# Kernel tuning notes

Hardware: AMD Instinct MI355X
Metric: run time of the kernel (lower is better)

Reference implementation:

```python
import jax, jax.numpy as jnp
import numpy as np

EPS = 1e-8

def div_small(a, b):
    b_safe = b * (b > EPS) + (b <= EPS) * EPS
    return a / b_safe

def cos_full(q1h, q2h, w):
    # q1h [b,s1,h], q2h [b,s1_or_1,h], w [P,h] -> [b,s1,P]
    a = q1h[:, :, None, :] * w          # [b,s1,P,h]
    c = q2h[:, :, None, :] * w          # [b,s1|1,P,h]
    num = jnp.sum(a * c, axis=-1)
    den = jnp.maximum(jnp.linalg.norm(a, axis=-1) * jnp.linalg.norm(c, axis=-1), EPS)
    return num / den

def cos_maxpool(q1h, q2h, w):
    # q1h [b,s1,h], q2h [b,s2,h], w [P,h] -> max over s2 of cosine -> [b,s1,P]
    a = q1h[:, :, None, :] * w          # [b,s1,P,h]
    c = q2h[:, :, None, :] * w          # [b,s2,P,h]
    num = jnp.einsum('biph,bjph->bijp', a, c)            # [b,s1,s2,P]
    na = jnp.linalg.norm(a, axis=-1)                     # [b,s1,P]
    nc = jnp.linalg.norm(c, axis=-1)                     # [b,s2,P]
    den = jnp.maximum(na[:, :, None, :] * nc[:, None, :, :], EPS)
    return jnp.max(num / den, axis=2)

def attention(q1, q2):
    # cosine-similarity matrix [b,s1,s2]
    n1 = jnp.linalg.norm(q1, axis=2, keepdims=True)      # [b,s1,1]
    n2 = jnp.linalg.norm(q2, axis=2, keepdims=True)      # [b,s2,1]
    num = jnp.einsum('bih,bjh->bij', q1, q2)
    return div_small(num, n1 * jnp.swapaxes(n2, 1, 2))

def setup_inputs() -> dict:
    key = jax.random.key(0)
    k1, k2, kw = jax.random.split(key, 3)
    q1_batch = jax.random.normal(k1, (16, 128, 512), dtype=jnp.float32)
    q2_batch = jax.random.normal(k2, (16, 128, 512), dtype=jnp.float32)
    W = jax.random.normal(kw, (8, 16, 256), dtype=jnp.float32)
    return {"q1_batch": q1_batch, "q2_batch": q2_batch, "W": W}

def reference(q1_batch, q2_batch, W):
    h = q1_batch.shape[-1] // 2
    q1_fw, q1_bw = q1_batch[..., :h], q1_batch[..., h:]
    q2_fw, q2_bw = q2_batch[..., :h], q2_batch[..., h:]

    # 1) full matching against last (fw) / first (bw) q2 state
    full_fw = cos_full(q1_fw, q2_fw[:, -1:, :], W[0])
    full_bw = cos_full(q1_bw, q2_bw[:, :1, :], W[1])

    # 2) max-pool matching over all q2 positions
    max_fw = cos_maxpool(q1_fw, q2_fw, W[2])
    max_bw = cos_maxpool(q1_bw, q2_bw, W[3])

    # 3) attentive matching
    att_fw = attention(q1_fw, q2_fw)                     # [b,s1,s2]
    att_bw = attention(q1_bw, q2_bw)
    at_q2_fw = att_fw[..., None] * q2_fw[:, None, :, :]  # [b,s1,s2,h]
    at_q2_bw = att_bw[..., None] * q2_bw[:, None, :, :]
    mean_fw = div_small(at_q2_fw.sum(axis=2), att_fw.sum(axis=2, keepdims=True))
    # NOTE: denominator intentionally uses att_fw (bug preserved from source)
    mean_bw = div_small(at_q2_bw.sum(axis=2), att_fw.sum(axis=2, keepdims=True))
    attn_fw = cos_full(q1_fw, mean_fw, W[4])
    attn_bw = cos_full(q1_bw, mean_bw, W[5])

    # 4) max-attentive matching
    max_at_fw = at_q2_fw.max(axis=2)                     # [b,s1,h]
    max_at_bw = at_q2_bw.max(axis=2)
    maxattn_fw = cos_full(q1_fw, max_at_fw, W[6])
    maxattn_bw = cos_full(q1_bw, max_at_bw, W[7])

    return jnp.concatenate(
        [full_fw, full_bw, max_fw, max_bw, attn_fw, attn_bw, maxattn_fw, maxattn_bw],
        axis=-1)
```

## Files before the change

kernel.cpp:

```cpp
#include <hip/hip_runtime.h>
#include <hip/hip_bf16.h>

#define B 16
#define L 128
#define H 256
#define H2 512
#define P 16
#define EPSF 1e-8f
#define LDSTR 72
#define PADQ 260
#define PATT 132

typedef __attribute__((ext_vector_type(8))) short short8;
typedef __attribute__((ext_vector_type(4))) short short4v;
typedef __attribute__((ext_vector_type(4))) float f32x4;

__device__ __forceinline__ short f2bf(float x) {
    unsigned u = __builtin_bit_cast(unsigned, x);
    u += 0x7fffu + ((u >> 16) & 1u);
    return (short)(u >> 16);
}
__device__ __forceinline__ float bf2f(short s) {
    unsigned u = ((unsigned)(unsigned short)s) << 16;
    return __builtin_bit_cast(float, u);
}

__global__ void __launch_bounds__(512) k_fused(
        const float* __restrict__ q1, const float* __restrict__ q2,
        const float* __restrict__ W, float* __restrict__ out) {
    int bd = blockIdx.x;
    int b = bd >> 1, dir = bd & 1;
    int m0 = blockIdx.y * 16;
    int t = threadIdx.x;
    int wave = t >> 6, l = t & 63, q = l >> 4, coll = l & 15;

    __shared__ __align__(16) short As[16 * LDSTR];
    __shared__ __align__(16) short Bs[128 * LDSTR];
    __shared__ __align__(16) float att_s[16][PATT];
    __shared__ __align__(16) float meanS[16][PADQ];
    __shared__ __align__(16) float maxS[16][PADQ];
    __shared__ __align__(16) float cful[256];
    __shared__ float nA[16], nB[128];

    const float* q1b = q1 + ((size_t)b * L + m0) * H2 + dir * H;
    const float* q2b = q2 + (size_t)b * L * H2 + dir * H;

    f32x4 acc = (f32x4){0.f, 0.f, 0.f, 0.f};
    float normA = 0.f, normB = 0.f;
    int arow = t >> 4, acol = (t & 15) * 4;
    int brow = t >> 2, bc0 = (t & 3) * 16;

    for (int kt = 0; kt < 4; kt++) {
        int k0 = kt * 64;
        if (t < 256) {
            float4 va = *(const float4*)(q1b + (size_t)arow * H2 + k0 + acol);
            normA += va.x * va.x + va.y * va.y + va.z * va.z + va.w * va.w;
            short4v sa = { f2bf(va.x), f2bf(va.y), f2bf(va.z), f2bf(va.w) };
            *(short4v*)(As + arow * LDSTR + acol) = sa;
        }
        for (int cc = 0; cc < 4; cc++) {
            float4 vb = *(const float4*)(q2b + (size_t)brow * H2 + k0 + bc0 + cc * 4);
            normB += vb.x * vb.x + vb.y * vb.y + vb.z * vb.z + vb.w * vb.w;
            short4v sb = { f2bf(vb.x), f2bf(vb.y), f2bf(vb.z), f2bf(vb.w) };
            *(short4v*)(Bs + brow * LDSTR + bc0 + cc * 4) = sb;
        }
        __syncthreads();
        for (int ks = 0; ks < 2; ks++) {
            int koff = ks * 32 + q * 8;
            short8 af = *(const short8*)(As + coll * LDSTR + koff);
            short8 bf = *(const short8*)(Bs + (wave * 16 + coll) * LDSTR + koff);
            acc = __builtin_amdgcn_mfma_f32_16x16x32_bf16(af, bf, acc, 0, 0, 0);
        }
        __syncthreads();
    }
    if (t < 256) {
        float sA = normA;
        for (int off = 1; off < 16; off <<= 1) sA += __shfl_xor(sA, off, 16);
        if ((t & 15) == 0) nA[arow] = sqrtf(sA);
    }
    {
        float sB = normB;
        sB += __shfl_xor(sB, 1, 4);
        sB += __shfl_xor(sB, 2, 4);
        if ((t & 3) == 0) nB[brow] = sqrtf(sB);
    }
    __syncthreads();
    {
        float n2 = nB[wave * 16 + coll];
        for (int r = 0; r < 4; r++) {
            float den = nA[q * 4 + r] * n2;
            den = den > EPSF ? den : EPSF;
            att_s[q * 4 + r][wave * 16 + coll] = acc[r] / den;
        }
    }
    if (t < 256) cful[t] = q2b[(size_t)(dir ? 0 : (L - 1)) * H2 + t];
    __syncthreads();

    int ig = t >> 6, hq = t & 63;
    int ia = ig * 2, ib = ia + 1;
    f32x4 s0 = (f32x4){0.f, 0.f, 0.f, 0.f}, s1 = s0;
    f32x4 mx0 = (f32x4){-INFINITY, -INFINITY, -INFINITY, -INFINITY}, mx1 = mx0;
    for (int j = 0; j < 128; j += 2) {
        float4 c0 = *(const float4*)(q2b + (size_t)j * H2 + hq * 4);
        float4 c1 = *(const float4*)(q2b + (size_t)(j + 1) * H2 + hq * 4);
        float wa0 = att_s[ia][j],     wb0 = att_s[ib][j];
        float wa1 = att_s[ia][j + 1], wb1 = att_s[ib][j + 1];
        f32x4 v0 = (f32x4){ wa0 * c0.x, wa0 * c0.y, wa0 * c0.z, wa0 * c0.w };
        f32x4 v1 = (f32x4){ wb0 * c0.x, wb0 * c0.y, wb0 * c0.z, wb0 * c0.w };
        f32x4 v2 = (f32x4){ wa1 * c1.x, wa1 * c1.y, wa1 * c1.z, wa1 * c1.w };
        f32x4 v3 = (f32x4){ wb1 * c1.x, wb1 * c1.y, wb1 * c1.z, wb1 * c1.w };
        s0 += v0; s0 += v2;
        s1 += v1; s1 += v3;
        mx0[0] = fmaxf(mx0[0], fmaxf(v0[0], v2[0]));
        mx0[1] = fmaxf(mx0[1], fmaxf(v0[1], v2[1]));
        mx0[2] = fmaxf(mx0[2], fmaxf(v0[2], v2[2]));
        mx0[3] = fmaxf(mx0[3], fmaxf(v0[3], v2[3]));
        mx1[0] = fmaxf(mx1[0], fmaxf(v1[0], v3[0]));
        mx1[1] = fmaxf(mx1[1], fmaxf(v1[1], v3[1]));
        mx1[2] = fmaxf(mx1[2], fmaxf(v1[2], v3[2]));
        mx1[3] = fmaxf(mx1[3], fmaxf(v1[3], v3[3]));
    }
    *(f32x4*)&meanS[ia][hq * 4] = s0;
    *(f32x4*)&meanS[ib][hq * 4] = s1;
    *(f32x4*)&maxS[ia][hq * 4] = mx0;
    *(f32x4*)&maxS[ib][hq * 4] = mx1;
    __syncthreads();

    int p3 = t >> 5, i3 = (t >> 1) & 15, half = t & 1;
    const float* a3 = q1b + (size_t)i3 * H2;
    for (int pc = 0; pc < 3; pc++) {
        int widx = (pc == 0) ? dir : (pc == 1 ? 4 + dir : 6 + dir);
        const float* crow = (pc == 0) ? cful
                           : (pc == 1 ? &meanS[i3][0] : &maxS[i3][0]);
        const float* wg = W + (size_t)widx * 4096 + p3 * 256;
        float num = 0.f, na = 0.f, nc = 0.f;
        for (int ch = 0; ch < 32; ch++) {
            int h = half * 128 + ch * 4;
            float4 a4 = *(const float4*)(a3 + h);
            f32x4 c4 = *(const f32x4*)(crow + h);
            float4 w4 = *(const float4*)(wg + h);
            float ws0 = w4.x * w4.x, ws1 = w4.y * w4.y;
            float ws2 = w4.z * w4.z, ws3 = w4.w * w4.w;
            num += a4.x * c4[0] * ws0;
            na  += a4.x * a4.x * ws0;
            nc  += c4[0] * c4[0] * ws0;
            num += a4.y * c4[1] * ws1;
            na  += a4.y * a4.y * ws1;
            nc  += c4[1] * c4[1] * ws1;
            num += a4.z * c4[2] * ws2;
            na  += a4.z * a4.z * ws2;
            nc  += c4[2] * c4[2] * ws2;
            num += a4.w * c4[3] * ws3;
            na  += a4.w * a4.w * ws3;
            nc  += c4[3] * c4[3] * ws3;
        }
        num += __shfl_xor(num, 1, 2);
        na  += __shfl_xor(na, 1, 2);
        nc  += __shfl_xor(nc, 1, 2);
        if (half == 0) {
            float den = sqrtf(na) * sqrtf(nc);
            den = den > EPSF ? den : EPSF;
            int colbase = (pc == 0 ? 0 : pc == 1 ? 64 : 96) + dir * 16;
            out[((size_t)b * L + m0 + i3) * 128 + colbase + p3] = num / den;
        }
    }
}

__global__ void __launch_bounds__(256, 2) k_maxpool_mfma(
        const float* __restrict__ q1, const float* __restrict__ q2,
        const float* __restrict__ W, float* __restrict__ out) {
    int bd = blockIdx.x;
    int b = bd >> 1, dir = bd & 1;
    int p = blockIdx.y;
    int t = threadIdx.x;

    __shared__ __align__(16) short As[128 * LDSTR];
    __shared__ __align__(16) short Bs[128 * LDSTR];
    __shared__ float wv[H];
    __shared__ float nrm[256];

    wv[t] = W[((size_t)(2 + dir) * P + p) * H + t];
    __syncthreads();

    f32x4 acc[2][8];
    for (int mt = 0; mt < 2; mt++)
        for (int nt = 0; nt < 8; nt++)
            acc[mt][nt] = (f32x4){0.f, 0.f, 0.f, 0.f};

    int lane16 = t & 15;
    int rgrp = t >> 4;
    int nrow = t & 127;
    int nmat = t >> 7;
    float normacc = 0.f;

    int wave = t >> 6;
    int l = t & 63;
    int q = l >> 4;
    int coll = l & 15;
    int m0 = wave * 32;

    const float* q1b = q1 + ((size_t)b * L) * H2 + dir * H;
    const float* q2b = q2 + ((size_t)b * L) * H2 + dir * H;

    for (int kt = 0; kt < 4; kt++) {
        int k0 = kt * 64;
        for (int pass = 0; pass < 8; pass++) {
            int row = rgrp + pass * 16;
            int c4 = lane16 * 4;
            float w0 = wv[k0 + c4], w1 = wv[k0 + c4 + 1];
            float w2 = wv[k0 + c4 + 2], w3 = wv[k0 + c4 + 3];
            float4 va = *(const float4*)(q1b + (size_t)row * H2 + k0 + c4);
            short4v sa = { f2bf(va.x * w0), f2bf(va.y * w1), f2bf(va.z * w2), f2bf(va.w * w3) };
            *(short4v*)(As + row * LDSTR + c4) = sa;
            float4 vb = *(const float4*)(q2b + (size_t)row * H2 + k0 + c4);
            short4v sb = { f2bf(vb.x * w0), f2bf(vb.y * w1), f2bf(vb.z * w2), f2bf(vb.w * w3) };
            *(short4v*)(Bs + row * LDSTR + c4) = sb;
        }
        __syncthreads();
        {
            const short* rowp = (nmat ? Bs : As) + nrow * LDSTR;
            for (int c = 0; c < 8; c++) {
                short8 s = *(const short8*)(rowp + c * 8);
                for (int jj = 0; jj < 8; jj++) {
                    float f = bf2f(s[jj]);
                    normacc += f * f;
                }
            }
        }
        for (int ks = 0; ks < 2; ks++) {
            int koff = ks * 32 + q * 8;
            short8 af0 = *(const short8*)(As + (m0 + coll) * LDSTR + koff);
            short8 af1 = *(const short8*)(As + (m0 + 16 + coll) * LDSTR + koff);
            for (int nt = 0; nt < 8; nt++) {
                short8 bfr = *(const short8*)(Bs + (nt * 16 + coll) * LDSTR + koff);
                acc[0][nt] = __builtin_amdgcn_mfma_f32_16x16x32_bf16(af0, bfr, acc[0][nt], 0, 0, 0);
                acc[1][nt] = __builtin_amdgcn_mfma_f32_16x16x32_bf16(af1, bfr, acc[1][nt], 0, 0, 0);
            }
        }
        __syncthreads();
    }
    nrm[t] = sqrtf(normacc);
    __syncthreads();

    float nav[2][4];
    for (int mt = 0; mt < 2; mt++)
        for (int r = 0; r < 4; r++)
            nav[mt][r] = nrm[m0 + mt * 16 + q * 4 + r];
    float rmax[2][4];
    for (int mt = 0; mt < 2; mt++)
        for (int r = 0; r < 4; r++) rmax[mt][r] = -INFINITY;
    for (int nt = 0; nt < 8; nt++) {
        float ncv = nrm[128 + nt * 16 + coll];
        for (int mt = 0; mt < 2; mt++)
            for (int r = 0; r < 4; r++) {
                float den = fmaxf(nav[mt][r] * ncv, EPSF);
                float v = acc[mt][nt][r] / den;
                rmax[mt][r] = fmaxf(rmax[mt][r], v);
            }
    }
    for (int off = 1; off < 16; off <<= 1)
        for (int mt = 0; mt < 2; mt++)
            for (int r = 0; r < 4; r++)
                rmax[mt][r] = fmaxf(rmax[mt][r], __shfl_xor(rmax[mt][r], off, 16));
    if (coll == 0) {
        for (int mt = 0; mt < 2; mt++)
            for (int r = 0; r < 4; r++) {
                int row = m0 + mt * 16 + q * 4 + r;
                out[((size_t)b * L + row) * 128 + 32 + dir * 16 + p] = rmax[mt][r];
            }
    }
}

extern "C" void kernel_launch(void* const* d_in, const int* in_sizes, int n_in,
                              void* d_out, int out_size, void* d_ws, size_t ws_size,
                              hipStream_t stream) {
    const float* q1 = (const float*)d_in[0];
    const float* q2 = (const float*)d_in[1];
    const float* W  = (const float*)d_in[2];
    float* out = (float*)d_out;
    (void)d_ws; (void)ws_size;

    k_fused<<<dim3(B * 2, 8), 512, 0, stream>>>(q1, q2, W, out);
    k_maxpool_mfma<<<dim3(B * 2, P), 256, 0, stream>>>(q1, q2, W, out);
}
```

Before: 126.3 us.

## Load q2 MFMA B fragments directly into registers, stage full q1 tile once

The attention GEMM no longer stages q2 through a shared-memory B tile across four K iterations with two barriers each. Each lane now loads its own B fragment straight from global memory into eight register short8 values and computes the q2 row norm with cross-lane shuffles. The whole q1 tile is converted to bf16 into shared memory once, so only a single barrier precedes the MFMA loop. This removes the LDS traffic and most of the syncs, at the cost of more registers per thread and less coalesced global loads for q2.

New measurement: 186.6 us. 47.7% more time.

```diff
diff --git a/kernel.cpp b/kernel.cpp
--- a/kernel.cpp
+++ b/kernel.cpp
@@ -8,6 +8,7 @@
 #define P 16
 #define EPSF 1e-8f
 #define LDSTR 72
+#define ASTR 264
 #define PADQ 260
 #define PATT 132
 
@@ -34,66 +35,65 @@
     int t = threadIdx.x;
     int wave = t >> 6, l = t & 63, q = l >> 4, coll = l & 15;
 
-    __shared__ __align__(16) short As[16 * LDSTR];
-    __shared__ __align__(16) short Bs[128 * LDSTR];
+    __shared__ __align__(16) short As[16 * ASTR];
     __shared__ __align__(16) float att_s[16][PATT];
     __shared__ __align__(16) float meanS[16][PADQ];
     __shared__ __align__(16) float maxS[16][PADQ];
     __shared__ __align__(16) float cful[256];
-    __shared__ float nA[16], nB[128];
+    __shared__ float nA[16];
 
     const float* q1b = q1 + ((size_t)b * L + m0) * H2 + dir * H;
     const float* q2b = q2 + (size_t)b * L * H2 + dir * H;
 
-    f32x4 acc = (f32x4){0.f, 0.f, 0.f, 0.f};
-    float normA = 0.f, normB = 0.f;
+    float normA = 0.f;
     int arow = t >> 4, acol = (t & 15) * 4;
-    int brow = t >> 2, bc0 = (t & 3) * 16;
-
     for (int kt = 0; kt < 4; kt++) {
-        int k0 = kt * 64;
         if (t < 256) {
+            int k0 = kt * 64;
             float4 va = *(const float4*)(q1b + (size_t)arow * H2 + k0 + acol);
             normA += va.x * va.x + va.y * va.y + va.z * va.z + va.w * va.w;
             short4v sa = { f2bf(va.x), f2bf(va.y), f2bf(va.z), f2bf(va.w) };
-            *(short4v*)(As + arow * LDSTR + acol) = sa;
-        }
-        for (int cc = 0; cc < 4; cc++) {
-            float4 vb = *(const float4*)(q2b + (size_t)brow * H2 + k0 + bc0 + cc * 4);
-            normB += vb.x * vb.x + vb.y * vb.y + vb.z * vb.z + vb.w * vb.w;
-            short4v sb = { f2bf(vb.x), f2bf(vb.y), f2bf(vb.z), f2bf(vb.w) };
-            *(short4v*)(Bs + brow * LDSTR + bc0 + cc * 4) = sb;
-        }
-        __syncthreads();
-        for (int ks = 0; ks < 2; ks++) {
-            int koff = ks * 32 + q * 8;
-            short8 af = *(const short8*)(As + coll * LDSTR + koff);
-            short8 bf = *(const short8*)(Bs + (wave * 16 + coll) * LDSTR + koff);
-            acc = __builtin_amdgcn_mfma_f32_16x16x32_bf16(af, bf, acc, 0, 0, 0);
-        }
-        __syncthreads();
+            *(short4v*)(As + arow * ASTR + k0 + acol) = sa;
+        }
     }
     if (t < 256) {
         float sA = normA;
         for (int off = 1; off < 16; off <<= 1) sA += __shfl_xor(sA, off, 16);
         if ((t & 15) == 0) nA[arow] = sqrtf(sA);
+        cful[t] = q2b[(size_t)(dir ? 0 : (L - 1)) * H2 + t];
+    }
+
+    int j0 = wave * 16 + coll;
+    const float* bro = q2b + (size_t)j0 * H2 + q * 8;
+    short8 bfrag[8];
+    float normB = 0.f;
+    for (int ks = 0; ks < 8; ks++) {
+        float4 u0 = *(const float4*)(bro + ks * 32);
+        float4 u1 = *(const float4*)(bro + ks * 32 + 4);
+        normB += u0.x * u0.x + u0.y * u0.y + u0.z * u0.z + u0.w * u0.w
+               + u1.x * u1.x + u1.y * u1.y + u1.z * u1.z + u1.w * u1.w;
+        short8 s = { f2bf(u0.x), f2bf(u0.y), f2bf(u0.z), f2bf(u0.w),
+                     f2bf(u1.x), f2bf(u1.y), f2bf(u1.z), f2bf(u1.w) };
+        bfrag[ks] = s;
+    }
+    normB += __shfl_xor(normB, 16, 64);
+    normB += __shfl_xor(normB, 32, 64);
+    float nBj = sqrtf(normB);
+
+    __syncthreads();
+
+    f32x4 acc = (f32x4){0.f, 0.f, 0.f, 0.f};
+    for (int ks = 0; ks < 8; ks++) {
+        short8 af = *(const short8*)(As + coll * ASTR + ks * 32 + q * 8);
+        acc = __builtin_amdgcn_mfma_f32_16x16x32_bf16(af, bfrag[ks], acc, 0, 0, 0);
     }
     {
-        float sB = normB;
-        sB += __shfl_xor(sB, 1, 4);
-        sB += __shfl_xor(sB, 2, 4);
-        if ((t & 3) == 0) nB[brow] = sqrtf(sB);
-    }
-    __syncthreads();
-    {
-        float n2 = nB[wave * 16 + coll];
         for (int r = 0; r < 4; r++) {
-            float den = nA[q * 4 + r] * n2;
+            float den = nA[q * 4 + r] * nBj;
             den = den > EPSF ? den : EPSF;
-            att_s[q * 4 + r][wave * 16 + coll] = acc[r] / den;
-        }
-    }
-    if (t < 256) cful[t] = q2b[(size_t)(dir ? 0 : (L - 1)) * H2 + t];
+            att_s[q * 4 + r][j0] = acc[r] / den;
+        }
+    }
     __syncthreads();
 
     int ig = t >> 6, hq = t & 63;
```
